# Kernel optimization log

Measured on AMD Instinct MI355X. Metric: run time of the kernel, lower is better.

## Reference

```python
import jax, jax.numpy as jnp
import numpy as np

N_NODES = 50000
N_EDGES = 800000
DIM = 64
N_ETYPES = 4
N_STEPS = 5


def setup_inputs() -> dict:
    key = jax.random.key(0)
    ks = jax.random.split(key, 10)
    feat = jax.random.normal(ks[0], (N_NODES, DIM), dtype=jnp.float32)
    src = jax.random.randint(ks[1], (N_EDGES,), 0, N_NODES, dtype=jnp.int32)
    dst = jax.random.randint(ks[2], (N_EDGES,), 0, N_NODES, dtype=jnp.int32)
    etypes = jax.random.randint(ks[3], (N_EDGES,), 0, N_ETYPES, dtype=jnp.int32)
    # per-edge-type Linear weights, xavier_normal with relu gain, zero bias
    gain = float(np.sqrt(2.0))
    std = gain * float(np.sqrt(2.0 / (DIM + DIM)))
    W = jax.random.normal(ks[4], (N_ETYPES, DIM, DIM), dtype=jnp.float32) * std  # [T, out, in]
    b = jnp.zeros((N_ETYPES, DIM), dtype=jnp.float32)
    # GRUCell params (torch layout: [3*dim, dim], gates order r,z,n), uniform(-1/sqrt(dim), 1/sqrt(dim))
    bound = 1.0 / float(np.sqrt(DIM))
    w_ih = jax.random.uniform(ks[5], (3 * DIM, DIM), minval=-bound, maxval=bound, dtype=jnp.float32)
    w_hh = jax.random.uniform(ks[6], (3 * DIM, DIM), minval=-bound, maxval=bound, dtype=jnp.float32)
    b_ih = jax.random.uniform(ks[7], (3 * DIM,), minval=-bound, maxval=bound, dtype=jnp.float32)
    b_hh = jax.random.uniform(ks[8], (3 * DIM,), minval=-bound, maxval=bound, dtype=jnp.float32)
    return {"feat": feat, "W": W, "b": b, "w_ih": w_ih, "w_hh": w_hh,
            "b_ih": b_ih, "b_hh": b_hh, "src": src, "dst": dst, "etypes": etypes}


def _gru_cell(a, h, w_ih, w_hh, b_ih, b_hh):
    gi = a @ w_ih.T + b_ih  # [N, 3*D]
    gh = h @ w_hh.T + b_hh
    i_r, i_z, i_n = jnp.split(gi, 3, axis=-1)
    h_r, h_z, h_n = jnp.split(gh, 3, axis=-1)
    r = jax.nn.sigmoid(i_r + h_r)
    z = jax.nn.sigmoid(i_z + h_z)
    n = jnp.tanh(i_n + r * h_n)
    return (1.0 - z) * n + z * h


def reference(feat, W, b, w_ih, w_hh, b_ih, b_hh, src, dst, etypes):
    n_nodes = feat.shape[0]
    h = feat
    for _ in range(N_STEPS):
        # apply every etype linear to all nodes: [N, T, D]
        h_all = jnp.einsum('nd,ted->nte', h, W) + b
        # per-edge message selects src node under its edge type: [E, D]
        m = h_all[src, etypes]
        # scatter-sum to destination nodes: [N, D]
        a = jax.ops.segment_sum(m, dst, num_segments=n_nodes)
        h = _gru_cell(a, h, w_ih, w_hh, b_ih, b_hh)
    return h
```

## Files before the change

kernel.cpp:

```cpp
#include <hip/hip_runtime.h>
#include <hip/hip_bf16.h>
#include <cstdint>

#define DIM 64
#define NSTEPS 5
#define HS  68
#define GLDH 194
#define SW  288
#define MAXVDEG 28

typedef __attribute__((ext_vector_type(8))) short short8v;
typedef __attribute__((ext_vector_type(4))) float f32x4;
typedef __attribute__((ext_vector_type(8))) _Float16 half8v;

__device__ __forceinline__ float sigmoidf_(float x){ return 1.0f/(1.0f+expf(-x)); }

__device__ __forceinline__ unsigned short f2bf(float x){
  unsigned u = __builtin_bit_cast(unsigned, x);
  return (unsigned short)((u + 0x7FFFu + ((u>>16)&1u)) >> 16);
}
__device__ __forceinline__ float bf2f(unsigned short b){
  unsigned u = ((unsigned)b)<<16;
  return __builtin_bit_cast(float, u);
}

__device__ __forceinline__ void splitbf8(const float* __restrict__ p,
                                         short8v& hi, short8v& lo){
  float4 x0 = *(const float4*)p;
  float4 x1 = *(const float4*)(p+4);
  float xs[8] = {x0.x,x0.y,x0.z,x0.w,x1.x,x1.y,x1.z,x1.w};
#pragma unroll
  for(int i=0;i<8;i++){
    unsigned short hb = f2bf(xs[i]);
    float rem = xs[i] - bf2f(hb);
    hi[i] = (short)hb;
    lo[i] = (short)f2bf(rem);
  }
}

__global__ __launch_bounds__(256) void k_pack(const float* __restrict__ src,
    short* __restrict__ ph, short* __restrict__ pl, int ncoltiles){
  int idx = blockIdx.x*256 + threadIdx.x;
  int total = ncoltiles*1024;
  if (idx >= total) return;
  int e = idx & 7, lane = (idx>>3)&63, kc = (idx>>9)&1, ct = idx>>10;
  int col = ct*16 + (lane&15);
  int k = kc*32 + (lane>>4)*8 + e;
  float v = src[(size_t)col*DIM + k];
  unsigned short hb = f2bf(v);
  ph[idx] = (short)hb;
  pl[idx] = (short)f2bf(v - bf2f(hb));
}

__global__ __launch_bounds__(256) void k_pack256(const float* __restrict__ W,
    const float* __restrict__ b, _Float16* __restrict__ ph, _Float16* __restrict__ pl){
  int idx = blockIdx.x*256 + threadIdx.x;
  if (idx >= 4*9*512) return;
  int e = idx & 7, lane = (idx>>3)&63, r = idx>>9;
  int kc = r % 9, ct = r / 9;
  int col = ct*16 + (lane&15);
  int k = kc*32 + (lane>>4)*8 + e;
  float v = 0.0f;
  if (k < 256){ int t = k>>6, d = k&63; v = W[(size_t)(t*64+col)*DIM + d]; }
  else if (k < 260){ v = b[(size_t)(k-256)*DIM + col]; }
  _Float16 hv = (_Float16)v;
  ph[idx] = hv;
  pl[idx] = (_Float16)(v - (float)hv);
}

__global__ __launch_bounds__(256) void k_cast(const float* __restrict__ x,
                                              _Float16* __restrict__ y, int n4){
  int i = blockIdx.x*256 + threadIdx.x;
  if (i >= n4) return;
  float4 v = *(const float4*)(x + (size_t)i*4);
  y[(size_t)i*4+0] = (_Float16)v.x; y[(size_t)i*4+1] = (_Float16)v.y;
  y[(size_t)i*4+2] = (_Float16)v.z; y[(size_t)i*4+3] = (_Float16)v.w;
}

__global__ __launch_bounds__(256) void k_scatter_vell(
    const int* __restrict__ src, const int* __restrict__ dst,
    const int* __restrict__ et, int* __restrict__ deg4,
    int* __restrict__ ell, int n_edges) {
  int e = blockIdx.x * 256 + threadIdx.x;
  if (e >= n_edges) return;
  int vn = dst[e]*4 + et[e];
  int rank = atomicAdd(&deg4[vn], 1);
  if (rank < MAXVDEG)
    ell[(size_t)vn * MAXVDEG + rank] = src[e];
}

__global__ __launch_bounds__(256) void k_gather(
    const _Float16* __restrict__ hb, const int* __restrict__ ell,
    const int* __restrict__ deg4, _Float16* __restrict__ s, int n_vnodes){
  int gid = blockIdx.x*256 + threadIdx.x;
  int vn = gid >> 3;
  if (vn >= n_vnodes) return;
  int q = gid & 7;
  int dg = min(deg4[vn], MAXVDEG);
  const int* ebase = ell + (size_t)vn * MAXVDEG;
  float acc[8] = {0,0,0,0,0,0,0,0};
  int i = 0;
  for (; i + 3 < dg; i += 4) {
    int4 p = *(const int4*)(ebase + i);
    half8v v0 = *(const half8v*)(hb + (size_t)p.x*DIM + q*8);
    half8v v1 = *(const half8v*)(hb + (size_t)p.y*DIM + q*8);
    half8v v2 = *(const half8v*)(hb + (size_t)p.z*DIM + q*8);
    half8v v3 = *(const half8v*)(hb + (size_t)p.w*DIM + q*8);
#pragma unroll
    for (int k=0;k<8;k++)
      acc[k] += ((float)v0[k] + (float)v1[k]) + ((float)v2[k] + (float)v3[k]);
  }
  for (; i < dg; ++i) {
    int sx = ebase[i];
    half8v v0 = *(const half8v*)(hb + (size_t)sx*DIM + q*8);
#pragma unroll
    for (int k=0;k<8;k++) acc[k] += (float)v0[k];
  }
  int n = vn >> 2, t = vn & 3;
  half8v out;
#pragma unroll
  for (int k=0;k<8;k++) out[k] = (_Float16)acc[k];
  *(half8v*)(s + (size_t)n*SW + t*DIM + q*8) = out;
  if (q == 0) s[(size_t)n*SW + 256 + t] = (_Float16)dg;
}

__global__ __launch_bounds__(256) void k_step(
    const _Float16* __restrict__ s, _Float16* __restrict__ hb,
    float* __restrict__ h,
    const _Float16* __restrict__ pw_h, const _Float16* __restrict__ pw_l,
    const short* __restrict__ pih_h, const short* __restrict__ pih_l,
    const short* __restrict__ phh_h, const short* __restrict__ phh_l,
    const float* __restrict__ b_ih, const float* __restrict__ b_hh,
    int n_nodes, int write_hb){
  __shared__ __align__(16) char smem[12416 + 4352];
  _Float16* stile = (_Float16*)smem;
  _Float16* gbuf  = (_Float16*)smem;
  float (*abuf)[HS] = (float(*)[HS])(smem + 12416);

  const int tid = threadIdx.x;
  const int wave = tid >> 6, lane = tid & 63;
  const int n0 = blockIdx.x * 16;
  if (n0 >= n_nodes) return;

  for (int t = tid; t < 576; t += 256)
    *(half8v*)(stile + t*8) = *(const half8v*)(s + (size_t)n0*SW + t*8);
  __syncthreads();

  const int rr = (lane >> 4) * 4;
  const int cc = lane & 15;
  {
    const int koff = (lane >> 4) * 8;
    const int arow = lane & 15;
    f32x4 acc4 = {0.f,0.f,0.f,0.f};
#pragma unroll
    for (int kc = 0; kc < 9; ++kc){
      half8v ah = *(const half8v*)(stile + arow*SW + kc*32 + koff);
      const half8v bh = *(const half8v*)(pw_h + ((size_t)(wave*9+kc)*64 + lane)*8);
      const half8v bl = *(const half8v*)(pw_l + ((size_t)(wave*9+kc)*64 + lane)*8);
      acc4 = __builtin_amdgcn_mfma_f32_16x16x32_f16(ah, bh, acc4, 0,0,0);
      acc4 = __builtin_amdgcn_mfma_f32_16x16x32_f16(ah, bl, acc4, 0,0,0);
    }
    __syncthreads();
#pragma unroll
    for (int q=0;q<4;q++) abuf[rr+q][wave*16 + cc] = acc4[q];
  }
  __syncthreads();

  const bool is_h = wave >= 2;
  const short* __restrict__ pbh = is_h ? phh_h : pih_h;
  const short* __restrict__ pbl = is_h ? phh_l : pih_l;
  const float* __restrict__ bv  = is_h ? b_hh : b_ih;
  _Float16* outb = gbuf + (is_h ? 16*GLDH : 0);

  const int kb = (lane >> 4) * 8;
  short8v ah0,al0,ah1,al1;
  if (is_h) {
    const float* xp = h + (size_t)(n0 + (lane & 15))*DIM;
    splitbf8(xp + kb,      ah0, al0);
    splitbf8(xp + 32 + kb, ah1, al1);
  } else {
    const float* xp = &abuf[lane & 15][0];
    splitbf8(xp + kb,      ah0, al0);
    splitbf8(xp + 32 + kb, ah1, al1);
  }

  const int ct0 = (wave & 1) * 6;
#pragma unroll
  for (int i = 0; i < 6; ++i){
    int ct = ct0 + i;
    const short8v bh0 = *(const short8v*)(pbh + ((size_t)(ct*2+0)*64 + lane)*8);
    const short8v bh1 = *(const short8v*)(pbh + ((size_t)(ct*2+1)*64 + lane)*8);
    const short8v bl0 = *(const short8v*)(pbl + ((size_t)(ct*2+0)*64 + lane)*8);
    const short8v bl1 = *(const short8v*)(pbl + ((size_t)(ct*2+1)*64 + lane)*8);
    float bias = bv[ct*16 + cc];
    f32x4 acc = {bias,bias,bias,bias};
    acc = __builtin_amdgcn_mfma_f32_16x16x32_bf16(ah0, bh0, acc, 0,0,0);
    acc = __builtin_amdgcn_mfma_f32_16x16x32_bf16(ah1, bh1, acc, 0,0,0);
    acc = __builtin_amdgcn_mfma_f32_16x16x32_bf16(al0, bh0, acc, 0,0,0);
    acc = __builtin_amdgcn_mfma_f32_16x16x32_bf16(al1, bh1, acc, 0,0,0);
    acc = __builtin_amdgcn_mfma_f32_16x16x32_bf16(ah0, bl0, acc, 0,0,0);
    acc = __builtin_amdgcn_mfma_f32_16x16x32_bf16(ah1, bl1, acc, 0,0,0);
#pragma unroll
    for (int q=0;q<4;q++)
      outb[(rr+q)*GLDH + ct*16 + cc] = (_Float16)acc[q];
  }
  __syncthreads();

#pragma unroll
  for (int it=0; it<4; ++it){
    int t = it*256 + tid;
    int j = t >> 6, d = t & 63;
    float gir = (float)gbuf[j*GLDH + d];
    float giz = (float)gbuf[j*GLDH + 64 + d];
    float gin = (float)gbuf[j*GLDH + 128 + d];
    float ghr = (float)gbuf[16*GLDH + j*GLDH + d];
    float ghz = (float)gbuf[16*GLDH + j*GLDH + 64 + d];
    float ghn = (float)gbuf[16*GLDH + j*GLDH + 128 + d];
    float r  = sigmoidf_(gir + ghr);
    float z  = sigmoidf_(giz + ghz);
    float nv = tanhf    (gin + r*ghn);
    size_t off = (size_t)(n0+j)*DIM + d;
    float ho = h[off];
    float hn = (1.0f - z)*nv + z*ho;
    h[off] = hn;
    if (write_hb) hb[off] = (_Float16)hn;
  }
}

extern "C" void kernel_launch(void* const* d_in, const int* in_sizes, int n_in,
                              void* d_out, int out_size, void* d_ws, size_t ws_size,
                              hipStream_t stream) {
  const float* feat = (const float*)d_in[0];
  const float* W    = (const float*)d_in[1];
  const float* b    = (const float*)d_in[2];
  const float* w_ih = (const float*)d_in[3];
  const float* w_hh = (const float*)d_in[4];
  const float* b_ih = (const float*)d_in[5];
  const float* b_hh = (const float*)d_in[6];
  const int* src = (const int*)d_in[7];
  const int* dst = (const int*)d_in[8];
  const int* et  = (const int*)d_in[9];

  const int n_nodes = in_sizes[0] / DIM;
  const int n_edges = in_sizes[7];
  const int n_vnodes = n_nodes * 4;

  float* h = (float*)d_out;
  char* ws = (char*)d_ws;
  _Float16* hb = (_Float16*)ws;  ws += (size_t)n_nodes * DIM * sizeof(_Float16);
  _Float16* s  = (_Float16*)ws;  ws += (size_t)n_nodes * SW * sizeof(_Float16);
  int* ell  = (int*)ws;   ws += (size_t)n_vnodes * MAXVDEG * sizeof(int);
  int* deg4 = (int*)ws;   ws += (size_t)n_vnodes * sizeof(int);
  _Float16* pw_h = (_Float16*)ws;  ws += 18432 * sizeof(_Float16);
  _Float16* pw_l = (_Float16*)ws;  ws += 18432 * sizeof(_Float16);
  short* pih_h = (short*)ws;  ws += 12288 * sizeof(short);
  short* pih_l = (short*)ws;  ws += 12288 * sizeof(short);
  short* phh_h = (short*)ws;  ws += 12288 * sizeof(short);
  short* phh_l = (short*)ws;  ws += 12288 * sizeof(short);

  hipMemcpyAsync(h, feat, (size_t)n_nodes * DIM * sizeof(float),
                 hipMemcpyDeviceToDevice, stream);

  k_pack256<<<72, 256, 0, stream>>>(W, b, pw_h, pw_l);
  k_pack<<<48, 256, 0, stream>>>(w_ih, pih_h, pih_l, 12);
  k_pack<<<48, 256, 0, stream>>>(w_hh, phh_h, phh_l, 12);
  k_cast<<<(n_nodes*DIM/4 + 255)/256, 256, 0, stream>>>(feat, hb, n_nodes*DIM/4);
  hipMemsetAsync(s, 0, (size_t)n_nodes * SW * sizeof(_Float16), stream);

  const int nblk_edges = (n_edges + 255) / 256;
  hipMemsetAsync(deg4, 0, (size_t)n_vnodes * sizeof(int), stream);
  k_scatter_vell<<<nblk_edges, 256, 0, stream>>>(src, dst, et, deg4, ell, n_edges);

  const int ggrid  = (n_vnodes * 8 + 255) / 256;
  const int rtiles = (n_nodes + 15) / 16;

  for (int st = 0; st < NSTEPS; ++st) {
    k_gather<<<ggrid, 256, 0, stream>>>(hb, ell, deg4, s, n_vnodes);
    k_step<<<rtiles, 256, 0, stream>>>(s, hb, h,
                                       pw_h, pw_l, pih_h, pih_l, phh_h, phh_l,
                                       b_ih, b_hh, n_nodes,
                                       (st < NSTEPS - 1) ? 1 : 0);
  }
}
```

Measured before the change: 344.3 us.

## Split neighbor gather by source half with 16-bit ELL indices

Edges are now bucketed by whether the source node falls in the lower or upper half of the node range. The lower half fills each per-(node,type) ELL row from the front and the upper half fills it from the back, and indices are stored as 16-bit values. Each step runs two gather kernels, each touching only half of the fp16 feature table, which is meant to keep that working set cache-resident and to halve index traffic. The second pass does a read-modify-write of the aggregate buffer and also writes the degree and zero padding, so the full memset of that buffer is dropped. The cost is an extra launch per step and a shared 32-slot row that could overlap if a row's combined degree exceeds 32.

```diff
diff --git a/kernel.cpp b/kernel.cpp
--- a/kernel.cpp
+++ b/kernel.cpp
@@ -7,7 +7,7 @@
 #define HS  68
 #define GLDH 194
 #define SW  288
-#define MAXVDEG 28
+#define VW  32
 
 typedef __attribute__((ext_vector_type(8))) short short8v;
 typedef __attribute__((ext_vector_type(4))) float f32x4;
@@ -79,33 +79,38 @@
 
 __global__ __launch_bounds__(256) void k_scatter_vell(
     const int* __restrict__ src, const int* __restrict__ dst,
-    const int* __restrict__ et, int* __restrict__ deg4,
-    int* __restrict__ ell, int n_edges) {
+    const int* __restrict__ et, int* __restrict__ degA, int* __restrict__ degB,
+    unsigned short* __restrict__ ell, int n_edges, int halfn) {
   int e = blockIdx.x * 256 + threadIdx.x;
   if (e >= n_edges) return;
   int vn = dst[e]*4 + et[e];
-  int rank = atomicAdd(&deg4[vn], 1);
-  if (rank < MAXVDEG)
-    ell[(size_t)vn * MAXVDEG + rank] = src[e];
-}
-
-__global__ __launch_bounds__(256) void k_gather(
-    const _Float16* __restrict__ hb, const int* __restrict__ ell,
-    const int* __restrict__ deg4, _Float16* __restrict__ s, int n_vnodes){
+  int sx = src[e];
+  if (sx < halfn) {
+    int r = atomicAdd(&degA[vn], 1);
+    if (r < VW) ell[(size_t)vn*VW + r] = (unsigned short)sx;
+  } else {
+    int r = atomicAdd(&degB[vn], 1);
+    if (r < VW) ell[(size_t)vn*VW + (VW-1) - r] = (unsigned short)sx;
+  }
+}
+
+__global__ __launch_bounds__(256) void k_gather_f(
+    const _Float16* __restrict__ hb, const unsigned short* __restrict__ ell,
+    const int* __restrict__ degA, _Float16* __restrict__ s, int n_vnodes){
   int gid = blockIdx.x*256 + threadIdx.x;
   int vn = gid >> 3;
   if (vn >= n_vnodes) return;
   int q = gid & 7;
-  int dg = min(deg4[vn], MAXVDEG);
-  const int* ebase = ell + (size_t)vn * MAXVDEG;
+  int dg = min(degA[vn], VW);
+  const unsigned short* ebase = ell + (size_t)vn * VW;
   float acc[8] = {0,0,0,0,0,0,0,0};
   int i = 0;
   for (; i + 3 < dg; i += 4) {
-    int4 p = *(const int4*)(ebase + i);
-    half8v v0 = *(const half8v*)(hb + (size_t)p.x*DIM + q*8);
-    half8v v1 = *(const half8v*)(hb + (size_t)p.y*DIM + q*8);
-    half8v v2 = *(const half8v*)(hb + (size_t)p.z*DIM + q*8);
-    half8v v3 = *(const half8v*)(hb + (size_t)p.w*DIM + q*8);
+    int s0=ebase[i], s1=ebase[i+1], s2=ebase[i+2], s3=ebase[i+3];
+    half8v v0 = *(const half8v*)(hb + (size_t)s0*DIM + q*8);
+    half8v v1 = *(const half8v*)(hb + (size_t)s1*DIM + q*8);
+    half8v v2 = *(const half8v*)(hb + (size_t)s2*DIM + q*8);
+    half8v v3 = *(const half8v*)(hb + (size_t)s3*DIM + q*8);
 #pragma unroll
     for (int k=0;k<8;k++)
       acc[k] += ((float)v0[k] + (float)v1[k]) + ((float)v2[k] + (float)v3[k]);
@@ -121,7 +126,46 @@
 #pragma unroll
   for (int k=0;k<8;k++) out[k] = (_Float16)acc[k];
   *(half8v*)(s + (size_t)n*SW + t*DIM + q*8) = out;
-  if (q == 0) s[(size_t)n*SW + 256 + t] = (_Float16)dg;
+}
+
+__global__ __launch_bounds__(256) void k_gather_b(
+    const _Float16* __restrict__ hb, const unsigned short* __restrict__ ell,
+    const int* __restrict__ degA, const int* __restrict__ degB,
+    _Float16* __restrict__ s, int n_vnodes){
+  int gid = blockIdx.x*256 + threadIdx.x;
+  int vn = gid >> 3;
+  if (vn >= n_vnodes) return;
+  int q = gid & 7;
+  int dgB = min(degB[vn], VW);
+  const unsigned short* ebase = ell + (size_t)vn * VW;
+  float acc[8] = {0,0,0,0,0,0,0,0};
+  int i = 0;
+  for (; i + 3 < dgB; i += 4) {
+    int s0=ebase[VW-1-i], s1=ebase[VW-2-i], s2=ebase[VW-3-i], s3=ebase[VW-4-i];
+    half8v v0 = *(const half8v*)(hb + (size_t)s0*DIM + q*8);
+    half8v v1 = *(const half8v*)(hb + (size_t)s1*DIM + q*8);
+    half8v v2 = *(const half8v*)(hb + (size_t)s2*DIM + q*8);
+    half8v v3 = *(const half8v*)(hb + (size_t)s3*DIM + q*8);
+#pragma unroll
+    for (int k=0;k<8;k++)
+      acc[k] += ((float)v0[k] + (float)v1[k]) + ((float)v2[k] + (float)v3[k]);
+  }
+  for (; i < dgB; ++i) {
+    int sx = ebase[VW-1-i];
+    half8v v0 = *(const half8v*)(hb + (size_t)sx*DIM + q*8);
+#pragma unroll
+    for (int k=0;k<8;k++) acc[k] += (float)v0[k];
+  }
+  int n = vn >> 2, t = vn & 3;
+  _Float16* sp = s + (size_t)n*SW + t*DIM + q*8;
+  half8v old = *(const half8v*)sp;
+  half8v out;
+#pragma unroll
+  for (int k=0;k<8;k++) out[k] = (_Float16)(acc[k] + (float)old[k]);
+  *(half8v*)sp = out;
+  if (q == 0) s[(size_t)n*SW + 256 + t] = (_Float16)(degA[vn] + degB[vn]);
+  int idx = t*8 + q;
+  if (idx < 28) s[(size_t)n*SW + 260 + idx] = (_Float16)0.0f;
 }
 
 __global__ __launch_bounds__(256) void k_step(
@@ -244,13 +288,16 @@
   const int n_nodes = in_sizes[0] / DIM;
   const int n_edges = in_sizes[7];
   const int n_vnodes = n_nodes * 4;
+  const int halfn = n_nodes / 2;
 
   float* h = (float*)d_out;
   char* ws = (char*)d_ws;
   _Float16* hb = (_Float16*)ws;  ws += (size_t)n_nodes * DIM * sizeof(_Float16);
   _Float16* s  = (_Float16*)ws;  ws += (size_t)n_nodes * SW * sizeof(_Float16);
-  int* ell  = (int*)ws;   ws += (size_t)n_vnodes * MAXVDEG * sizeof(int);
-  int* deg4 = (int*)ws;   ws += (size_t)n_vnodes * sizeof(int);
+  unsigned short* ell = (unsigned short*)ws;
+  ws += (size_t)n_vnodes * VW * sizeof(unsigned short);
+  int* degA = (int*)ws;   ws += (size_t)n_vnodes * sizeof(int);
+  int* degB = (int*)ws;   ws += (size_t)n_vnodes * sizeof(int);
   _Float16* pw_h = (_Float16*)ws;  ws += 18432 * sizeof(_Float16);
   _Float16* pw_l = (_Float16*)ws;  ws += 18432 * sizeof(_Float16);
   short* pih_h = (short*)ws;  ws += 12288 * sizeof(short);
@@ -265,17 +312,18 @@
   k_pack<<<48, 256, 0, stream>>>(w_ih, pih_h, pih_l, 12);
   k_pack<<<48, 256, 0, stream>>>(w_hh, phh_h, phh_l, 12);
   k_cast<<<(n_nodes*DIM/4 + 255)/256, 256, 0, stream>>>(feat, hb, n_nodes*DIM/4);
-  hipMemsetAsync(s, 0, (size_t)n_nodes * SW * sizeof(_Float16), stream);
 
   const int nblk_edges = (n_edges + 255) / 256;
-  hipMemsetAsync(deg4, 0, (size_t)n_vnodes * sizeof(int), stream);
-  k_scatter_vell<<<nblk_edges, 256, 0, stream>>>(src, dst, et, deg4, ell, n_edges);
+  hipMemsetAsync(degA, 0, (size_t)n_vnodes * 2 * sizeof(int), stream);
+  k_scatter_vell<<<nblk_edges, 256, 0, stream>>>(src, dst, et, degA, degB,
+                                                 ell, n_edges, halfn);
 
   const int ggrid  = (n_vnodes * 8 + 255) / 256;
   const int rtiles = (n_nodes + 15) / 16;
 
   for (int st = 0; st < NSTEPS; ++st) {
-    k_gather<<<ggrid, 256, 0, stream>>>(hb, ell, deg4, s, n_vnodes);
+    k_gather_f<<<ggrid, 256, 0, stream>>>(hb, ell, degA, s, n_vnodes);
+    k_gather_b<<<ggrid, 256, 0, stream>>>(hb, ell, degA, degB, s, n_vnodes);
     k_step<<<rtiles, 256, 0, stream>>>(s, hb, h,
                                        pw_h, pw_l, pih_h, pih_l, phh_h, phh_l,
                                        b_ih, b_hh, n_nodes,
```

New measurement: 409.7 us. 1.19x slower.
